# Kernel tuning notes

Measured on AMD Instinct MI355X. Metric: run time of the kernel, lower is better.

Reference implementation:

```python
import jax, jax.numpy as jnp
import numpy as np

B, C, F = 4096, 63, 250  # batch, EEG channels (nodes per sample), features
NEG_SLOPE = 0.2          # PyG GATConv default leaky-relu slope


def setup_inputs() -> dict:
    key = jax.random.key(0)
    kx, kw, ks, kd, kb = jax.random.split(key, 5)
    x = jax.random.normal(kx, (B, 1, C, F), dtype=jnp.float32)
    # GATConv params (heads=1): linear weight, att_src, att_dst, bias
    W = jax.random.normal(kw, (F, F), dtype=jnp.float32) * (1.0 / np.sqrt(F))
    att_src = jax.random.normal(ks, (F,), dtype=jnp.float32) * (1.0 / np.sqrt(F))
    att_dst = jax.random.normal(kd, (F,), dtype=jnp.float32) * (1.0 / np.sqrt(F))
    bias = jnp.zeros((F,), dtype=jnp.float32)
    # edge_index over first 63 nodes only (as in the original module), all i != j
    ii, jj = np.meshgrid(np.arange(C), np.arange(C), indexing='ij')
    mask = ii != jj
    base_src = ii[mask].astype(np.int32)  # [3906]
    base_dst = jj[mask].astype(np.int32)
    # PyG add_self_loops=True: self loop for every node in the stacked batch graph
    N = B * C
    loops = np.arange(N, dtype=np.int32)
    src = jnp.asarray(np.concatenate([base_src, loops]))
    dst = jnp.asarray(np.concatenate([base_dst, loops]))
    return {"x": x, "W": W, "att_src": att_src, "att_dst": att_dst,
            "bias": bias, "src": src, "dst": dst}


def reference(x, W, att_src, att_dst, bias, src, dst):
    b, _, c, f = x.shape
    N = b * c
    h = x.reshape(N, f) @ W                      # [N, F] transformed node features
    a_s = h @ att_src                            # [N] source attention logits
    a_d = h @ att_dst                            # [N] target attention logits
    e = jax.nn.leaky_relu(a_s[src] + a_d[dst], NEG_SLOPE)  # [E]
    # segment softmax over incoming edges of each target node
    m = jax.ops.segment_max(e, dst, num_segments=N)
    ex = jnp.exp(e - m[dst])
    denom = jax.ops.segment_sum(ex, dst, num_segments=N)
    alpha = ex / denom[dst]                      # [E]
    out = jax.ops.segment_sum(alpha[:, None] * h[src], dst, num_segments=N)
    out = out + bias
    return out.reshape(b, 1, c, f)
```

## Files before the change

### kernel.cpp

```cpp
#include <hip/hip_runtime.h>


#define FDIM   250
#define NROWS  258048
#define RPB    128
#define NBLK   (NROWS / RPB)

typedef __attribute__((ext_vector_type(8))) short  short8;
typedef __attribute__((ext_vector_type(4))) float  f32x4;

__device__ __forceinline__ unsigned short f2bf(float f) {
    unsigned u = __builtin_bit_cast(unsigned, f);
    u += 0x7fffu + ((u >> 16) & 1u);
    return (unsigned short)(u >> 16);
}

__global__ void wprep_kernel(const float* __restrict__ W, unsigned short* __restrict__ Wt) {
    int idx = blockIdx.x * 256 + threadIdx.x;
    int c   = idx >> 13;
    int rem = idx & 8191;
    int n   = rem >> 5;
    int k   = rem & 31;
    int kk  = c * 32 + k;
    float v = (kk < FDIM && n < FDIM) ? W[kk * FDIM + n] : 0.0f;
    Wt[idx] = f2bf(v);
}

__global__ __launch_bounds__(512, 4) void gemm_kernel(
    const float* __restrict__ x,
    const unsigned short* __restrict__ Wt,
    const float* __restrict__ bias,
    float* __restrict__ out,
    float* __restrict__ ws_h)
{
    __shared__ uint4 sB4[4096];
    char* sB = (char*)sB4;

    const int tid  = threadIdx.x;
    const int lane = tid & 63;
    const int wave = tid >> 6;
    const int m    = lane & 15;
    const int kg   = lane >> 4;

    const size_t row0 = (size_t)blockIdx.x * RPB + wave * 16;
    const float*  xr  = x + (row0 + m) * FDIM;
    const int bbase   = m * 64 + ((kg ^ ((m >> 1) & 3)) << 4);
    const uint4* Wt4  = (const uint4*)Wt;

    f32x4 acc[16];
#pragma unroll
    for (int i = 0; i < 16; ++i)
#pragma unroll
        for (int e = 0; e < 4; ++e) acc[i][e] = 0.0f;

    float2 a0[4], a1[4];

#define LOAD_A(dst, c) do {                                                   \
        const float* _p = xr + (c) * 32 + kg * 8;                             \
        if ((c) < 7 || kg < 3) {                                              \
            dst[0] = *(const float2*)_p;       dst[1] = *(const float2*)(_p + 2); \
            dst[2] = *(const float2*)(_p + 4); dst[3] = *(const float2*)(_p + 6); \
        } else {         \
            dst[0] = *(const float2*)_p;                                      \
            dst[1] = make_float2(0.f, 0.f);                                   \
            dst[2] = make_float2(0.f, 0.f);                                   \
            dst[3] = make_float2(0.f, 0.f);                                   \
        }                                                                     \
    } while (0)

#define STAGE(h) do {                                                         \
        _Pragma("unroll")                                                     \
        for (int t = 0; t < 8; ++t) {                                         \
            int g  = t * 512 + tid;             \
            int cl = g >> 10, rr = g & 1023;                                  \
            int nn = rr >> 2, ks = rr & 3;                                    \
            uint4 v = Wt4[(h) * 4096 + g];                                    \
            *(uint4*)(sB + cl * 16384 + nn * 64 + ((ks ^ ((nn >> 1) & 3)) << 4)) = v; \
        }                                                                     \
    } while (0)

#define COMPUTE(buf, c) do {                                                  \
        short8 afrag;                                                         \
        afrag[0] = (short)f2bf(buf[0].x); afrag[1] = (short)f2bf(buf[0].y);   \
        afrag[2] = (short)f2bf(buf[1].x); afrag[3] = (short)f2bf(buf[1].y);   \
        afrag[4] = (short)f2bf(buf[2].x); afrag[5] = (short)f2bf(buf[2].y);   \
        afrag[6] = (short)f2bf(buf[3].x); afrag[7] = (short)f2bf(buf[3].y);   \
        const char* _bb = sB + ((c) & 3) * 16384 + bbase;                     \
        _Pragma("unroll")                                                     \
        for (int nt = 0; nt < 16; ++nt) {                                     \
            short8 bfrag = *(const short8*)(_bb + nt * 1024);                 \
            acc[nt] = __builtin_amdgcn_mfma_f32_16x16x32_bf16(afrag, bfrag, acc[nt], 0, 0, 0); \
        }                                                                     \
    } while (0)

    STAGE(0);
    LOAD_A(a0, 0);
    LOAD_A(a1, 1);
    __syncthreads();

    COMPUTE(a0, 0); LOAD_A(a0, 2);
    COMPUTE(a1, 1); LOAD_A(a1, 3);
    COMPUTE(a0, 2); LOAD_A(a0, 4);
    COMPUTE(a1, 3); LOAD_A(a1, 5);

    __syncthreads();
    STAGE(1);
    __syncthreads();

    COMPUTE(a0, 4); LOAD_A(a0, 6);
    COMPUTE(a1, 5); LOAD_A(a1, 7);
    COMPUTE(a0, 6);
    COMPUTE(a1, 7);

#undef LOAD_A
#undef STAGE
#undef COMPUTE

    const int r0 = kg * 4;
#pragma unroll
    for (int nt = 0; nt < 16; ++nt) {
        int col = nt * 16 + m;
        if (col < FDIM) {
            float bv = bias[col];
#pragma unroll
            for (int r = 0; r < 4; ++r) {
                size_t row = row0 + r0 + r;
                float v = acc[nt][r];
                out[row * FDIM + col] = v + bv;
                if (row < 63) ws_h[row * FDIM + col] = v;
            }
        }
    }
}

__global__ __launch_bounds__(256) void attn_kernel(
    const float* __restrict__ h,
    const float* __restrict__ att_src,
    const float* __restrict__ att_dst,
    const float* __restrict__ bias,
    float* __restrict__ out)
{
    const int j = blockIdx.x;
    const int tid = threadIdx.x;

    __shared__ float s_as[63];
    __shared__ float s_ad;
    __shared__ float s_alpha[63];
    __shared__ float s_inv;

    if (tid < 63) {
        float a = 0.f;
        #pragma unroll 5
        for (int f = 0; f < FDIM; ++f) a += h[tid * FDIM + f] * att_src[f];
        s_as[tid] = a;
    } else if (tid == 63) {
        float a = 0.f;
        #pragma unroll 5
        for (int f = 0; f < FDIM; ++f) a += h[j * FDIM + f] * att_dst[f];
        s_ad = a;
    }
    __syncthreads();

    if (tid == 0) {
        float m = -1e30f;
        for (int i = 0; i < 63; ++i) {
            float v = s_as[i] + s_ad;
            v = (v >= 0.f) ? v : 0.2f * v;
            s_alpha[i] = v;
            m = fmaxf(m, v);
        }
        float d = 0.f;
        for (int i = 0; i < 63; ++i) {
            float ex = __expf(s_alpha[i] - m);
            s_alpha[i] = ex;
            d += ex;
        }
        s_inv = 1.0f / d;
    }
    __syncthreads();

    if (tid < FDIM) {
        float a = 0.f;
        #pragma unroll
        for (int i = 0; i < 63; ++i) a += s_alpha[i] * h[i * FDIM + tid];
        out[j * FDIM + tid] = a * s_inv + bias[tid];
    }
}

extern "C" void kernel_launch(void* const* d_in, const int* in_sizes, int n_in,
                              void* d_out, int out_size, void* d_ws, size_t ws_size,
                              hipStream_t stream) {
    const float* x       = (const float*)d_in[0];
    const float* W       = (const float*)d_in[1];
    const float* att_src = (const float*)d_in[2];
    const float* att_dst = (const float*)d_in[3];
    const float* bias    = (const float*)d_in[4];

    float* out = (float*)d_out;

    unsigned short* Wt = (unsigned short*)d_ws;
    float* ws_h = (float*)((char*)d_ws + 131072);

    wprep_kernel<<<256, 256, 0, stream>>>(W, Wt);
    gemm_kernel<<<NBLK, 512, 0, stream>>>(x, Wt, bias, out, ws_h);
    attn_kernel<<<63, 256, 0, stream>>>(ws_h, att_src, att_dst, bias, out);
}
```

Baseline: 516.1 us.

## Make GEMM persistent with register-resident W and double-buffered LDS A tiles

The GEMM kernel becomes persistent, with a fixed grid of 512 blocks looping over 16-row tiles. Each wave holds its slice of bf16 W (32 output columns) in registers for the whole kernel, where before W was restaged into LDS by every block. The x tiles are loaded coalesced as float4, converted to bf16, and written into double-buffered padded LDS while the next tile's global loads are issued ahead of time. The aim is to remove the repeated W staging traffic and overlap x loads with MFMA work, at the cost of a barrier per tile and more register pressure.

```diff
diff --git a/kernel.cpp b/kernel.cpp
--- a/kernel.cpp
+++ b/kernel.cpp
@@ -1,10 +1,13 @@
 #include <hip/hip_runtime.h>
 
 
-#define FDIM   250
-#define NROWS  258048
-#define RPB    128
-#define NBLK   (NROWS / RPB)
+#define FDIM    250
+#define NROWS   258048
+#define TR      16
+#define NTILES  (NROWS / TR)
+#define GRID    512
+#define RSTRIDE 560
+#define BUFB    (TR * RSTRIDE)
 
 typedef __attribute__((ext_vector_type(8))) short  short8;
 typedef __attribute__((ext_vector_type(4))) float  f32x4;
@@ -33,8 +36,7 @@
     float* __restrict__ out,
     float* __restrict__ ws_h)
 {
-    __shared__ uint4 sB4[4096];
-    char* sB = (char*)sB4;
+    __shared__ char sA[2 * BUFB];
 
     const int tid  = threadIdx.x;
     const int lane = tid & 63;
@@ -42,95 +44,117 @@
     const int m    = lane & 15;
     const int kg   = lane >> 4;
 
-    const size_t row0 = (size_t)blockIdx.x * RPB + wave * 16;
-    const float*  xr  = x + (row0 + m) * FDIM;
-    const int bbase   = m * 64 + ((kg ^ ((m >> 1) & 3)) << 4);
-    const uint4* Wt4  = (const uint4*)Wt;
-
-    f32x4 acc[16];
+    const int cn0 = wave * 32 + m;
+    const int cn1 = cn0 + 16;
+    const bool ok1 = cn1 < FDIM;
+    short8 bfr0[8], bfr1[8];
 #pragma unroll
-    for (int i = 0; i < 16; ++i)
-#pragma unroll
-        for (int e = 0; e < 4; ++e) acc[i][e] = 0.0f;
-
-    float2 a0[4], a1[4];
-
-#define LOAD_A(dst, c) do {                                                   \
-        const float* _p = xr + (c) * 32 + kg * 8;                             \
-        if ((c) < 7 || kg < 3) {                                              \
-            dst[0] = *(const float2*)_p;       dst[1] = *(const float2*)(_p + 2); \
-            dst[2] = *(const float2*)(_p + 4); dst[3] = *(const float2*)(_p + 6); \
-        } else {         \
-            dst[0] = *(const float2*)_p;                                      \
-            dst[1] = make_float2(0.f, 0.f);                                   \
-            dst[2] = make_float2(0.f, 0.f);                                   \
-            dst[3] = make_float2(0.f, 0.f);                                   \
+    for (int c = 0; c < 8; ++c) {
+        bfr0[c] = *(const short8*)(Wt + ((size_t)(c * 256 + cn0) * 32 + kg * 8));
+        bfr1[c] = *(const short8*)(Wt + ((size_t)(c * 256 + cn1) * 32 + kg * 8));
+    }
+    const float bv0 = bias[cn0];
+    const float bv1 = ok1 ? bias[cn1] : 0.0f;
+
+    if (tid < 480) {
+        int r2 = tid / 15;
+        int d  = tid - r2 * 15;
+        *(unsigned*)(sA + r2 * RSTRIDE + 500 + 4 * d) = 0u;
+    }
+
+    float4 rA[2];
+
+#define LOADS(t) do {                                                         \
+        const float4* _xp = (const float4*)x + (size_t)(t) * 1000;            \
+        _Pragma("unroll")                                                     \
+        for (int q = 0; q < 2; ++q) {                                         \
+            int s = q * 512 + tid;                                            \
+            if (s < 1000) rA[q] = _xp[s];                                     \
         }                                                                     \
     } while (0)
 
-#define STAGE(h) do {                                                         \
+#define CVTWRITE(bsel) do {                                                   \
         _Pragma("unroll")                                                     \
-        for (int t = 0; t < 8; ++t) {                                         \
-            int g  = t * 512 + tid;             \
-            int cl = g >> 10, rr = g & 1023;                                  \
-            int nn = rr >> 2, ks = rr & 3;                                    \
-            uint4 v = Wt4[(h) * 4096 + g];                                    \
-            *(uint4*)(sB + cl * 16384 + nn * 64 + ((ks ^ ((nn >> 1) & 3)) << 4)) = v; \
+        for (int q = 0; q < 2; ++q) {                                         \
+            int s = q * 512 + tid;                                            \
+            if (s < 1000) {                                                   \
+                float4 v = rA[q];                                             \
+                _Pragma("unroll")                                             \
+                for (int p = 0; p < 2; ++p) {                                 \
+                    int fp  = 4 * s + 2 * p;                                  \
+                    int row = fp / 250;                                       \
+                    int col = fp - row * 250;                \
+                    float e0 = p ? v.z : v.x;                                 \
+                    float e1 = p ? v.w : v.y;                                 \
+                    unsigned u = (unsigned)f2bf(e0) | ((unsigned)f2bf(e1) << 16); \
+                    *(unsigned*)(sA + (bsel) * BUFB + row * RSTRIDE + col * 2) = u; \
+                }                                                             \
+            }                                                                 \
         }                                                                     \
     } while (0)
 
-#define COMPUTE(buf, c) do {                                                  \
-        short8 afrag;                                                         \
-        afrag[0] = (short)f2bf(buf[0].x); afrag[1] = (short)f2bf(buf[0].y);   \
-        afrag[2] = (short)f2bf(buf[1].x); afrag[3] = (short)f2bf(buf[1].y);   \
-        afrag[4] = (short)f2bf(buf[2].x); afrag[5] = (short)f2bf(buf[2].y);   \
-        afrag[6] = (short)f2bf(buf[3].x); afrag[7] = (short)f2bf(buf[3].y);   \
-        const char* _bb = sB + ((c) & 3) * 16384 + bbase;                     \
-        _Pragma("unroll")                                                     \
-        for (int nt = 0; nt < 16; ++nt) {                                     \
-            short8 bfrag = *(const short8*)(_bb + nt * 1024);                 \
-            acc[nt] = __builtin_amdgcn_mfma_f32_16x16x32_bf16(afrag, bfrag, acc[nt], 0, 0, 0); \
-        }                                                                     \
+#define BARRIER() do {                                                        \
+        asm volatile("s_waitcnt lgkmcnt(0)" ::: "memory");                    \
+        __builtin_amdgcn_s_barrier();                                         \
+        __builtin_amdgcn_sched_barrier(0);                                    \
     } while (0)
 
-    STAGE(0);
-    LOAD_A(a0, 0);
-    LOAD_A(a1, 1);
-    __syncthreads();
-
-    COMPUTE(a0, 0); LOAD_A(a0, 2);
-    COMPUTE(a1, 1); LOAD_A(a1, 3);
-    COMPUTE(a0, 2); LOAD_A(a0, 4);
-    COMPUTE(a1, 3); LOAD_A(a1, 5);
-
-    __syncthreads();
-    STAGE(1);
-    __syncthreads();
-
-    COMPUTE(a0, 4); LOAD_A(a0, 6);
-    COMPUTE(a1, 5); LOAD_A(a1, 7);
-    COMPUTE(a0, 6);
-    COMPUTE(a1, 7);
-
-#undef LOAD_A
-#undef STAGE
-#undef COMPUTE
-
-    const int r0 = kg * 4;
+    int tile  = blockIdx.x;
+    bool have = tile < NTILES;
+    if (have) {
+        LOADS(tile);
+        CVTWRITE(0);
+    }
+    int nextt  = tile + GRID;
+    bool haveN = nextt < NTILES;
+    if (haveN) LOADS(nextt);
+    BARRIER();
+
+    int buf = 0;
+    while (have) {
+        f32x4 acc0 = {0.f, 0.f, 0.f, 0.f};
+        f32x4 acc1 = {0.f, 0.f, 0.f, 0.f};
+        const char* ab = sA + buf * BUFB + m * RSTRIDE;
 #pragma unroll
-    for (int nt = 0; nt < 16; ++nt) {
-        int col = nt * 16 + m;
-        if (col < FDIM) {
-            float bv = bias[col];
+        for (int c = 0; c < 8; ++c) {
+            short8 a = *(const short8*)(ab + c * 64 + kg * 16);
+            acc0 = __builtin_amdgcn_mfma_f32_16x16x32_bf16(a, bfr0[c], acc0, 0, 0, 0);
+            acc1 = __builtin_amdgcn_mfma_f32_16x16x32_bf16(a, bfr1[c], acc1, 0, 0, 0);
+        }
+
+        const size_t trow0 = (size_t)tile * TR;
+        const bool spill = trow0 < 63;
+        const int rb = kg * 4;
 #pragma unroll
-            for (int r = 0; r < 4; ++r) {
-                size_t row = row0 + r0 + r;
-                float v = acc[nt][r];
-                out[row * FDIM + col] = v + bv;
-                if (row < 63) ws_h[row * FDIM + col] = v;
+        for (int r = 0; r < 4; ++r) {
+            size_t row = trow0 + rb + r;
+            float v0 = acc0[r];
+            out[row * FDIM + cn0] = v0 + bv0;
+            if (ok1) {
+                float v1 = acc1[r];
+                out[row * FDIM + cn1] = v1 + bv1;
+                if (spill && row < 63) ws_h[row * FDIM + cn1] = v1;
             }
-        }
-    }
+            if (spill && row < 63) ws_h[row * FDIM + cn0] = v0;
+        }
+
+        if (haveN) {
+            CVTWRITE(buf ^ 1);
+            int t2 = nextt + GRID;
+            if (t2 < NTILES) LOADS(t2);
+        }
+        BARRIER();
+
+        tile  = nextt;
+        nextt += GRID;
+        have  = haveN;
+        haveN = nextt < NTILES;
+        buf  ^= 1;
+    }
+
+#undef LOADS
+#undef CVTWRITE
+#undef BARRIER
 }
 
 __global__ __launch_bounds__(256) void attn_kernel(
@@ -202,6 +226,6 @@
     float* ws_h = (float*)((char*)d_ws + 131072);
 
     wprep_kernel<<<256, 256, 0, stream>>>(W, Wt);
-    gemm_kernel<<<NBLK, 512, 0, stream>>>(x, Wt, bias, out, ws_h);
+    gemm_kernel<<<GRID, 512, 0, stream>>>(x, Wt, bias, out, ws_h);
     attn_kernel<<<63, 256, 0, stream>>>(ws_h, att_src, att_dst, bias, out);
 }
```

After: 466.3 us. 9.7% less time.
